# Kernel tuning notes

Hardware: AMD Instinct MI355X
Metric: run time of the kernel (lower is better)

## Reference

```python
import jax, jax.numpy as jnp
import numpy as np

N = 6144       # nodes
E = 12288      # edges (~2N for a sparse simplicial complex)
NF = 32        # node features
EF = 16        # edge features
NH = [32, 32]  # node_hidden
EH = [16, 16]  # edge_hidden
EPS = 1e-5


def setup_inputs() -> dict:
    key = jax.random.key(0)
    ks = jax.random.split(key, 24)
    s = 0.1  # weight init scale
    inp = {}
    inp["X_n"] = jax.random.normal(ks[0], (N, NF), jnp.float32)
    inp["X_e"] = jax.random.normal(ks[1], (E, EF), jnp.float32)
    # normalized adjacency-like operator (non-negative, row mass ~1)
    inp["A_tilde"] = jax.random.uniform(ks[2], (N, N), jnp.float32) * (1.0 / N)
    # normalized Hodge-1 Laplacian-like operator
    inp["L1_tilde"] = jax.random.normal(ks[3], (E, E), jnp.float32) * (1.0 / np.sqrt(E))
    # incidence-like operator
    inp["B1"] = jax.random.normal(ks[4], (N, E), jnp.float32) * (1.0 / np.sqrt(E))
    # GNN linear layers: weight [out, in] (torch convention)
    inp["gnn_W0"] = jax.random.normal(ks[5], (NH[0], NF), jnp.float32) * s
    inp["gnn_b0"] = jnp.zeros((NH[0],), jnp.float32)
    inp["gnn_W1"] = jax.random.normal(ks[6], (NH[1], NH[0]), jnp.float32) * s
    inp["gnn_b1"] = jnp.zeros((NH[1],), jnp.float32)
    # HoSC layer 0: theta in=EF out=EH[0], BN params
    inp["th_W0"] = jax.random.normal(ks[7], (EH[0], EF), jnp.float32) * s
    inp["th_b0"] = jnp.zeros((EH[0],), jnp.float32)
    inp["bn_g0"] = jnp.ones((EH[0],), jnp.float32)
    inp["bn_b0"] = jnp.zeros((EH[0],), jnp.float32)
    # HoSC layer 1: input collapses to 1 channel (max keepdim)
    inp["th_W1"] = jax.random.normal(ks[8], (EH[1], 1), jnp.float32) * s
    inp["th_b1"] = jnp.zeros((EH[1],), jnp.float32)
    inp["bn_g1"] = jnp.ones((EH[1],), jnp.float32)
    inp["bn_b1"] = jnp.zeros((EH[1],), jnp.float32)
    # head: fc1 in = NH[-1] + len(EH) = 34, out = 2N; fc2 out = 1
    inp["fc1_W"] = jax.random.normal(ks[9], (2 * N, NH[-1] + len(EH)), jnp.float32) * s
    inp["fc1_b"] = jnp.zeros((2 * N,), jnp.float32)
    inp["fc2_W"] = jax.random.normal(ks[10], (1, 2 * N), jnp.float32) * s
    inp["fc2_b"] = jnp.zeros((1,), jnp.float32)
    return inp


def _gnn_layer(A, H, W, b):
    # H <- relu((A @ H) @ W^T + b)
    return jax.nn.relu(jnp.matmul(jnp.matmul(A, H), W.T) + b)


def _hosc_layer(Z, L1, W, b, g, beta):
    Zt = jnp.matmul(Z, W.T) + b            # theta
    Zc = jnp.matmul(L1, Zt)                # Laplacian conv
    m = jnp.mean(Zc, axis=0)               # BatchNorm1d (training-mode batch stats)
    v = jnp.var(Zc, axis=0)
    Zp = jax.nn.relu(g * (Zc - m) * jax.lax.rsqrt(v + EPS) + beta)
    return jnp.max(Zp, axis=1, keepdims=True)  # [E, 1]


def reference(X_n, X_e, A_tilde, L1_tilde, B1,
              gnn_W0, gnn_b0, gnn_W1, gnn_b1,
              th_W0, th_b0, bn_g0, bn_b0,
              th_W1, th_b1, bn_g1, bn_b1,
              fc1_W, fc1_b, fc2_W, fc2_b):
    # GNN over nodes
    H = _gnn_layer(A_tilde, X_n, gnn_W0, gnn_b0)
    H_n = _gnn_layer(A_tilde, H, gnn_W1, gnn_b1)      # [N, NH[-1]]
    # HoSC over edges
    Z0 = _hosc_layer(X_e, L1_tilde, th_W0, th_b0, bn_g0, bn_b0)  # [E, 1]
    Z1 = _hosc_layer(Z0, L1_tilde, th_W1, th_b1, bn_g1, bn_b1)   # [E, 1]
    Z_cat = jnp.concatenate([Z0, Z1], axis=1)         # [E, 2]
    H_e = jnp.matmul(B1, Z_cat)                       # [N, 2]
    # head
    Hcat = jnp.concatenate([H_n, H_e], axis=1)        # [N, 34]
    f = jax.nn.relu(jnp.matmul(Hcat, fc1_W.T) + fc1_b)
    f = jnp.matmul(f, fc2_W.T) + fc2_b                # [N, 1]
    return jax.nn.sigmoid(f).squeeze(-1)              # [N]
```

## Files before the change

### kernel.cpp

```cpp
#include <hip/hip_runtime.h>
#include <hip/hip_cooperative_groups.h>
#include <math.h>

namespace cg = cooperative_groups;

#define NND 6144
#define NED 12288
#define GRID 512
static constexpr float EPS_BN = 1e-5f;

#define HN_OFF    0
#define HE_OFF    196608
#define ST_OFF    208896
#define Y_OFF     208960
#define T0_OFF    405568
#define T1_OFF    602176
#define Z0_OFF    798784
#define Z1_OFF    811072
#define U_OFF     823360
#define S_OFF     835648
#define PP_OFF    847936

typedef float floatx4 __attribute__((ext_vector_type(4)));

__device__ __forceinline__ float4 ntload4(const float* p) {
  floatx4 v = __builtin_nontemporal_load(reinterpret_cast<const floatx4*>(p));
  return make_float4(v.x, v.y, v.z, v.w);
}
__device__ __forceinline__ float4 ld4(const float* p) {
  return *reinterpret_cast<const float4*>(p);
}
__device__ __forceinline__ void gll16(const float* g, float* l) {
  __builtin_amdgcn_global_load_lds(
      (const __attribute__((address_space(1))) unsigned int*)g,
      (__attribute__((address_space(3))) unsigned int*)l, 16, 0, 0);
}

struct Params {
  const float *X_n, *X_e, *A, *L1, *B1;
  const float *gW0, *gb0, *gW1, *gb1;
  const float *tW0, *tb0, *bng0, *bnb0;
  const float *tW1, *tb1, *bng1, *bnb1;
  const float *fc1W, *fc1b, *fc2W, *fc2b;
  float *ws;
  float *out;
};

template<int PHASE>
__global__ __launch_bounds__(256, 2) void pipeline(Params p) {
  __shared__ float lds[12288];
  float* sst = &lds[12032];
  float* red = &lds[12064];

  const int tid  = threadIdx.x;
  const int lane = tid & 63;
  const int w    = tid >> 6;
  const int blk  = blockIdx.x;
  const int gtid = blk * 256 + tid;
  constexpr bool ALL = (PHASE == 0);

  float* Hn = p.ws + HN_OFF;
  float* he = p.ws + HE_OFF;
  float* st = p.ws + ST_OFF;
  float* Y  = p.ws + Y_OFF;
  float* T0 = p.ws + T0_OFF;
  float* T1 = p.ws + T1_OFF;
  float* Z0 = p.ws + Z0_OFF;
  float* Z1 = p.ws + Z1_OFF;
  float* u  = p.ws + U_OFF;
  float* s  = p.ws + S_OFF;
  float* pp = p.ws + PP_OFF;

  auto gemm32 = [&](const float* bias, float* outp) {
    const int r0 = blk * 12;
    float acc[3][32];
    #pragma unroll
    for (int r = 0; r < 3; ++r)
      #pragma unroll
      for (int c = 0; c < 32; ++c) acc[r][c] = 0.f;

    for (int kb = 0; kb < NND; kb += 256) {
      #pragma unroll
      for (int i = 0; i < 8; ++i) {
        const int yr = w * 8 + i;
        gll16(Y + (size_t)yr * NND + kb + lane * 4, &lds[yr * 256]);
      }
      #pragma unroll
      for (int i = 0; i < 3; ++i) {
        const int ar = w * 3 + i;
        gll16(p.A + (size_t)(r0 + ar) * NND + kb + lane * 4, &lds[8192 + ar * 256]);
      }
      __syncthreads();
      float4 av[3];
      #pragma unroll
      for (int r = 0; r < 3; ++r)
        av[r] = ld4(&lds[8192 + (w * 3 + r) * 256 + lane * 4]);
      #pragma unroll
      for (int c = 0; c < 32; ++c) {
        const float4 y = ld4(&lds[c * 256 + lane * 4]);
        #pragma unroll
        for (int r = 0; r < 3; ++r) {
          acc[r][c] = fmaf(av[r].x, y.x, acc[r][c]);
          acc[r][c] = fmaf(av[r].y, y.y, acc[r][c]);
          acc[r][c] = fmaf(av[r].z, y.z, acc[r][c]);
          acc[r][c] = fmaf(av[r].w, y.w, acc[r][c]);
        }
      }
      __syncthreads();
    }
    #pragma unroll
    for (int r = 0; r < 3; ++r) {
      float wv[32];
      #pragma unroll
      for (int c = 0; c < 32; ++c)
        wv[c] = acc[r][c] + __shfl_xor(acc[r][c], 32, 64);
      #pragma unroll
      for (int b = 4; b >= 0; --b) {
        const int m = 1 << b;
        const bool hi = (lane & m) != 0;
        #pragma unroll
        for (int i = 0; i < (1 << b); ++i) {
          float x = wv[i], yv = wv[i + (1 << b)];
          float send = hi ? x : yv;
          float recv = __shfl_xor(send, m, 64);
          wv[i] = (hi ? yv : x) + recv;
        }
      }
      if (lane < 32) {
        float v = fmaxf(wv[0] + bias[lane], 0.f);
        outp[(size_t)(r0 + w * 3 + r) * 32 + lane] = v;
      }
    }
  };

  if constexpr (ALL || PHASE == 1) {
    if (blk == 0 && tid < 64) st[tid] = 0.f;
    if (gtid < NND) {
      const int m = gtid;
      float x[32];
      #pragma unroll
      for (int k = 0; k < 32; k += 4) {
        float4 v = ld4(p.X_n + (size_t)m * 32 + k);
        x[k] = v.x; x[k+1] = v.y; x[k+2] = v.z; x[k+3] = v.w;
      }
      #pragma unroll
      for (int oc = 0; oc < 32; ++oc) {
        float acc = 0.f;
        #pragma unroll
        for (int k = 0; k < 32; ++k) acc = fmaf(x[k], p.gW0[oc * 32 + k], acc);
        Y[(size_t)oc * NND + m] = acc;
      }
    } else if (gtid < NND + NED) {
      const int e = gtid - NND;
      float x[16];
      #pragma unroll
      for (int k = 0; k < 16; k += 4) {
        float4 v = ld4(p.X_e + (size_t)e * 16 + k);
        x[k] = v.x; x[k+1] = v.y; x[k+2] = v.z; x[k+3] = v.w;
      }
      #pragma unroll
      for (int oc = 0; oc < 16; ++oc) {
        float acc = p.tb0[oc];
        #pragma unroll
        for (int k = 0; k < 16; ++k) acc = fmaf(x[k], p.tW0[oc * 16 + k], acc);
        T1[(size_t)oc * NED + e] = acc;
      }
    }
  }
  if constexpr (ALL) cg::this_grid().sync();

  if constexpr (ALL || PHASE == 2) gemm32(p.gb0, T0);
  if constexpr (ALL) cg::this_grid().sync();

  if constexpr (ALL || PHASE == 3) {
    if (gtid < NND) {
      const int m = gtid;
      float x[32];
      #pragma unroll
      for (int k = 0; k < 32; k += 4) {
        float4 v = ld4(T0 + (size_t)m * 32 + k);
        x[k] = v.x; x[k+1] = v.y; x[k+2] = v.z; x[k+3] = v.w;
      }
      #pragma unroll
      for (int oc = 0; oc < 32; ++oc) {
        float acc = 0.f;
        #pragma unroll
        for (int k = 0; k < 32; ++k) acc = fmaf(x[k], p.gW1[oc * 32 + k], acc);
        Y[(size_t)oc * NND + m] = acc;
      }
    }
  }
  if constexpr (ALL) cg::this_grid().sync();

  if constexpr (ALL || PHASE == 4) gemm32(p.gb1, Hn);
  if constexpr (ALL) cg::this_grid().sync();

  if constexpr (ALL || PHASE == 5) {
    const int r0 = blk * 24;
    float acc[6][16];
    #pragma unroll
    for (int r = 0; r < 6; ++r)
      #pragma unroll
      for (int c = 0; c < 16; ++c) acc[r][c] = 0.f;

    for (int kb = 0; kb < NED; kb += 256) {
      #pragma unroll
      for (int i = 0; i < 4; ++i) {
        const int yr = w * 4 + i;
        gll16(T1 + (size_t)yr * NED + kb + lane * 4, &lds[yr * 256]);
      }
      #pragma unroll
      for (int i = 0; i < 6; ++i) {
        const int ar = w * 6 + i;
        gll16(p.L1 + (size_t)(r0 + ar) * NED + kb + lane * 4, &lds[4096 + ar * 256]);
      }
      __syncthreads();
      float4 av[6];
      #pragma unroll
      for (int r = 0; r < 6; ++r)
        av[r] = ld4(&lds[4096 + (w * 6 + r) * 256 + lane * 4]);
      #pragma unroll
      for (int c = 0; c < 16; ++c) {
        const float4 y = ld4(&lds[c * 256 + lane * 4]);
        #pragma unroll
        for (int r = 0; r < 6; ++r) {
          acc[r][c] = fmaf(av[r].x, y.x, acc[r][c]);
          acc[r][c] = fmaf(av[r].y, y.y, acc[r][c]);
          acc[r][c] = fmaf(av[r].z, y.z, acc[r][c]);
          acc[r][c] = fmaf(av[r].w, y.w, acc[r][c]);
        }
      }
      __syncthreads();
    }
    float stS = 0.f, stQ = 0.f;
    #pragma unroll
    for (int pr = 0; pr < 3; ++pr) {
      float wv[32];
      #pragma unroll
      for (int c = 0; c < 16; ++c) {
        wv[c]      = acc[2*pr][c]   + __shfl_xor(acc[2*pr][c], 32, 64);
        wv[16 + c] = acc[2*pr+1][c] + __shfl_xor(acc[2*pr+1][c], 32, 64);
      }
      #pragma unroll
      for (int b = 4; b >= 0; --b) {
        const int m = 1 << b;
        const bool hi = (lane & m) != 0;
        #pragma unroll
        for (int i = 0; i < (1 << b); ++i) {
          float x = wv[i], yv = wv[i + (1 << b)];
          float send = hi ? x : yv;
          float recv = __shfl_xor(send, m, 64);
          wv[i] = (hi ? yv : x) + recv;
        }
      }
      if (lane < 32) {
        const int rsel = lane >> 4, csel = lane & 15;
        const float v = wv[0];
        T0[(size_t)(r0 + w * 6 + pr * 2 + rsel) * 16 + csel] = v;
        stS += v; stQ += v * v;
      }
    }
    if (tid < 32) sst[tid] = 0.f;
    __syncthreads();
    if (lane < 32) {
      atomicAdd(&sst[lane & 15], stS);
      atomicAdd(&sst[16 + (lane & 15)], stQ);
    }
    __syncthreads();
    if (tid < 32) atomicAdd(st + tid, sst[tid]);
  }
  if constexpr (ALL) cg::this_grid().sync();

  if constexpr (ALL || PHASE == 6) {
    if (gtid < NED) {
      const int e = gtid;
      const float invE = 1.f / (float)NED;
      float best = -3.4e38f;
      #pragma unroll
      for (int c = 0; c < 16; ++c) {
        float m = st[c] * invE;
        float var = st[16 + c] * invE - m * m;
        float sc = p.bng0[c] * rsqrtf(var + EPS_BN);
        float sh = p.bnb0[c] - m * sc;
        best = fmaxf(best, fmaf(T0[(size_t)e * 16 + c], sc, sh));
      }
      Z0[e] = fmaxf(best, 0.f);
    }
  }
  if constexpr (ALL) cg::this_grid().sync();

  if constexpr (ALL || PHASE == 7) {
    const int rb = GRID - 1 - blk;
    const int r0 = rb * 24 + w * 6;
    const float* mp[6];
    #pragma unroll
    for (int r = 0; r < 6; ++r) mp[r] = p.L1 + (size_t)(r0 + r) * NED;
    float ua[6] = {0,0,0,0,0,0}, sa[6] = {0,0,0,0,0,0};
    float4 a[6], an[6];
    #pragma unroll
    for (int r = 0; r < 6; ++r) a[r] = ntload4(mp[r] + lane * 4);
    float4 z = ld4(Z0 + lane * 4), zn;
    for (int kb = 0; kb < NED; kb += 256) {
      const int k = kb + lane * 4;
      const bool more = (kb + 256) < NED;
      if (more) {
        #pragma unroll
        for (int r = 0; r < 6; ++r) an[r] = ntload4(mp[r] + k + 256);
        zn = ld4(Z0 + k + 256);
      }
      #pragma unroll
      for (int r = 0; r < 6; ++r) {
        ua[r] += a[r].x*z.x + a[r].y*z.y + a[r].z*z.z + a[r].w*z.w;
        sa[r] += a[r].x + a[r].y + a[r].z + a[r].w;
      }
      if (more) {
        #pragma unroll
        for (int r = 0; r < 6; ++r) a[r] = an[r];
        z = zn;
      }
    }
    #pragma unroll
    for (int r = 0; r < 6; ++r)
      #pragma unroll
      for (int m = 1; m < 64; m <<= 1) {
        ua[r] += __shfl_xor(ua[r], m, 64);
        sa[r] += __shfl_xor(sa[r], m, 64);
      }
    if (lane == 0) {
      float s1 = 0.f, s2 = 0.f, s3 = 0.f, s4 = 0.f, s5 = 0.f;
      #pragma unroll
      for (int r = 0; r < 6; ++r) {
        u[r0 + r] = ua[r]; s[r0 + r] = sa[r];
        s1 += ua[r]; s2 += sa[r];
        s3 += ua[r] * ua[r]; s4 += sa[r] * sa[r]; s5 += ua[r] * sa[r];
      }
      red[w * 5 + 0] = s1; red[w * 5 + 1] = s2; red[w * 5 + 2] = s3;
      red[w * 5 + 3] = s4; red[w * 5 + 4] = s5;
    }
    __syncthreads();
    if (tid < 5)
      atomicAdd(st + 32 + tid, red[tid] + red[5 + tid] + red[10 + tid] + red[15 + tid]);
  }
  if constexpr (ALL) cg::this_grid().sync();

  if constexpr (ALL || PHASE == 8) {
    if (gtid < NED) {
      const int e = gtid;
      const float invE = 1.f / (float)NED;
      const float Su = st[32], Ss = st[33], Suu = st[34], Sss = st[35], Sus = st[36];
      const float uu = u[e], ssv = s[e];
      float best = -3.4e38f;
      #pragma unroll
      for (int c = 0; c < 16; ++c) {
        const float wc = p.tW1[c], bc = p.tb1[c];
        const float mean = (wc * Su + bc * Ss) * invE;
        const float ex2 = (wc * wc * Suu + 2.f * wc * bc * Sus + bc * bc * Sss) * invE;
        const float var = ex2 - mean * mean;
        const float sc = p.bng1[c] * rsqrtf(var + EPS_BN);
        const float sh = p.bnb1[c] - mean * sc;
        best = fmaxf(best, fmaf(wc * uu + bc * ssv, sc, sh));
      }
      Z1[e] = fmaxf(best, 0.f);
    }
  }
  if constexpr (ALL) cg::this_grid().sync();

  if constexpr (ALL || PHASE == 9) {
    const int r0 = blk * 12 + w * 3;
    const float* mp[3];
    #pragma unroll
    for (int r = 0; r < 3; ++r) mp[r] = p.B1 + (size_t)(r0 + r) * NED;
    float uu[3] = {0,0,0}, vv[3] = {0,0,0};
    float4 a[3], an[3];
    #pragma unroll
    for (int r = 0; r < 3; ++r) a[r] = ntload4(mp[r] + lane * 4);
    float4 z = ld4(Z0 + lane * 4), y = ld4(Z1 + lane * 4), zn, yn;
    for (int kb = 0; kb < NED; kb += 256) {
      const int k = kb + lane * 4;
      const bool more = (kb + 256) < NED;
      if (more) {
        #pragma unroll
        for (int r = 0; r < 3; ++r) an[r] = ntload4(mp[r] + k + 256);
        zn = ld4(Z0 + k + 256); yn = ld4(Z1 + k + 256);
      }
      #pragma unroll
      for (int r = 0; r < 3; ++r) {
        uu[r] += a[r].x*z.x + a[r].y*z.y + a[r].z*z.z + a[r].w*z.w;
        vv[r] += a[r].x*y.x + a[r].y*y.y + a[r].z*y.z + a[r].w*y.w;
      }
      if (more) {
        #pragma unroll
        for (int r = 0; r < 3; ++r) a[r] = an[r];
        z = zn; y = yn;
      }
    }
    #pragma unroll
    for (int r = 0; r < 3; ++r)
      #pragma unroll
      for (int m = 1; m < 64; m <<= 1) {
        uu[r] += __shfl_xor(uu[r], m, 64);
        vv[r] += __shfl_xor(vv[r], m, 64);
      }
    if (lane == 0) {
      #pragma unroll
      for (int r = 0; r < 3; ++r) {
        he[(r0 + r) * 2]     = uu[r];
        he[(r0 + r) * 2 + 1] = vv[r];
      }
    }
  }
  if constexpr (ALL) cg::this_grid().sync();

  if constexpr (ALL || PHASE == 10) {
    const int nb = blk & 7, jb = blk >> 3;
    int n[3];
    float h[3][34];
    float acc[3] = {0.f, 0.f, 0.f};
    #pragma unroll
    for (int i = 0; i < 3; ++i) {
      n[i] = nb * 768 + i * 256 + tid;
      #pragma unroll
      for (int k = 0; k < 32; k += 4) {
        float4 v = ld4(Hn + (size_t)n[i] * 32 + k);
        h[i][k] = v.x; h[i][k+1] = v.y; h[i][k+2] = v.z; h[i][k+3] = v.w;
      }
      float2 e2 = *reinterpret_cast<const float2*>(he + n[i] * 2);
      h[i][32] = e2.x; h[i][33] = e2.y;
    }
    const int j0 = jb * 192;
    for (int j = j0; j < j0 + 192; ++j) {
      const float* wp = p.fc1W + (size_t)j * 34;
      const float bj = p.fc1b[j], vj = p.fc2W[j];
      float s0 = bj, s1 = bj, s2 = bj;
      #pragma unroll
      for (int k = 0; k < 34; ++k) {
        const float wk = wp[k];
        s0 = fmaf(h[0][k], wk, s0);
        s1 = fmaf(h[1][k], wk, s1);
        s2 = fmaf(h[2][k], wk, s2);
      }
      acc[0] += fmaxf(s0, 0.f) * vj;
      acc[1] += fmaxf(s1, 0.f) * vj;
      acc[2] += fmaxf(s2, 0.f) * vj;
    }
    #pragma unroll
    for (int i = 0; i < 3; ++i) pp[(size_t)jb * NND + n[i]] = acc[i];
  }
  if constexpr (ALL) cg::this_grid().sync();

  if constexpr (ALL || PHASE == 11) {
    if (gtid < NND) {
      float acc = 0.f;
      for (int j = 0; j < 64; ++j) acc += pp[(size_t)j * NND + gtid];
      p.out[gtid] = 1.f / (1.f + expf(-(acc + p.fc2b[0])));
    }
  }
}

extern "C" void kernel_launch(void* const* d_in, const int* in_sizes, int n_in,
                              void* d_out, int out_size, void* d_ws, size_t ws_size,
                              hipStream_t stream) {
  Params p;
  p.X_n  = (const float*)d_in[0];
  p.X_e  = (const float*)d_in[1];
  p.A    = (const float*)d_in[2];
  p.L1   = (const float*)d_in[3];
  p.B1   = (const float*)d_in[4];
  p.gW0  = (const float*)d_in[5];
  p.gb0  = (const float*)d_in[6];
  p.gW1  = (const float*)d_in[7];
  p.gb1  = (const float*)d_in[8];
  p.tW0  = (const float*)d_in[9];
  p.tb0  = (const float*)d_in[10];
  p.bng0 = (const float*)d_in[11];
  p.bnb0 = (const float*)d_in[12];
  p.tW1  = (const float*)d_in[13];
  p.tb1  = (const float*)d_in[14];
  p.bng1 = (const float*)d_in[15];
  p.bnb1 = (const float*)d_in[16];
  p.fc1W = (const float*)d_in[17];
  p.fc1b = (const float*)d_in[18];
  p.fc2W = (const float*)d_in[19];
  p.fc2b = (const float*)d_in[20];
  p.ws   = (float*)d_ws;
  p.out  = (float*)d_out;

  int maxBlk = 0;
  hipError_t oe = hipOccupancyMaxActiveBlocksPerMultiprocessor(
      &maxBlk, pipeline<0>, 256, 0);
  bool coop_ok = (oe == hipSuccess) && (maxBlk >= 2);

  if (coop_ok) {
    void* kargs[] = { &p };
    hipError_t le = hipLaunchCooperativeKernel(
        (const void*)&pipeline<0>, dim3(GRID), dim3(256), kargs, 0, stream);
    if (le == hipSuccess) return;
  }

  pipeline<1><<<GRID, 256, 0, stream>>>(p);
  pipeline<2><<<GRID, 256, 0, stream>>>(p);
  pipeline<3><<<GRID, 256, 0, stream>>>(p);
  pipeline<4><<<GRID, 256, 0, stream>>>(p);
  pipeline<5><<<GRID, 256, 0, stream>>>(p);
  pipeline<6><<<GRID, 256, 0, stream>>>(p);
  pipeline<7><<<GRID, 256, 0, stream>>>(p);
  pipeline<8><<<GRID, 256, 0, stream>>>(p);
  pipeline<9><<<GRID, 256, 0, stream>>>(p);
  pipeline<10><<<GRID, 256, 0, stream>>>(p);
  pipeline<11><<<GRID, 256, 0, stream>>>(p);
}
```

Baseline: 610.3 us.

## Double cooperative grid to 1024 blocks with four blocks per CU

Doubles the cooperative grid and raises the launch bound to four blocks per CU, shrinking LDS per block. Every phase's per-block work is re-split to match: the A GEMM splits columns across wave pairs, the L1 GEMM and row reductions take half the rows, and the head splits fc1 rows into 128 partial chunks. The goal is more waves in flight to hide memory latency in the bandwidth-bound matrix passes. In exchange, accumulators per thread drop to fit the register budget, the A GEMM reloads Y tiles per half-row-set with some idle waves, and the final reduction reads twice as many partial sums.

```diff
diff --git a/kernel.cpp b/kernel.cpp
--- a/kernel.cpp
+++ b/kernel.cpp
@@ -6,7 +6,7 @@
 
 #define NND 6144
 #define NED 12288
-#define GRID 512
+#define GRID 1024
 static constexpr float EPS_BN = 1e-5f;
 
 #define HN_OFF    0
@@ -47,10 +47,10 @@
 };
 
 template<int PHASE>
-__global__ __launch_bounds__(256, 2) void pipeline(Params p) {
-  __shared__ float lds[12288];
-  float* sst = &lds[12032];
-  float* red = &lds[12064];
+__global__ __launch_bounds__(256, 4) void pipeline(Params p) {
+  __shared__ float lds[10240];
+  float* sst = &lds[10176];
+  float* red = &lds[10208];
 
   const int tid  = threadIdx.x;
   const int lane = tid & 63;
@@ -72,12 +72,14 @@
   float* pp = p.ws + PP_OFF;
 
   auto gemm32 = [&](const float* bias, float* outp) {
-    const int r0 = blk * 12;
-    float acc[3][32];
+    const int rg = w >> 1, cg_ = w & 1;
+    const int r0 = blk * 6;
+    const int c0 = cg_ * 16;
+    float acc[3][16];
     #pragma unroll
     for (int r = 0; r < 3; ++r)
       #pragma unroll
-      for (int c = 0; c < 32; ++c) acc[r][c] = 0.f;
+      for (int c = 0; c < 16; ++c) acc[r][c] = 0.f;
 
     for (int kb = 0; kb < NND; kb += 256) {
       #pragma unroll
@@ -86,18 +88,19 @@
         gll16(Y + (size_t)yr * NND + kb + lane * 4, &lds[yr * 256]);
       }
       #pragma unroll
-      for (int i = 0; i < 3; ++i) {
-        const int ar = w * 3 + i;
-        gll16(p.A + (size_t)(r0 + ar) * NND + kb + lane * 4, &lds[8192 + ar * 256]);
+      for (int i = 0; i < 2; ++i) {
+        const int ar = w * 2 + i;
+        if (ar < 6)
+          gll16(p.A + (size_t)(r0 + ar) * NND + kb + lane * 4, &lds[8192 + ar * 256]);
       }
       __syncthreads();
       float4 av[3];
       #pragma unroll
       for (int r = 0; r < 3; ++r)
-        av[r] = ld4(&lds[8192 + (w * 3 + r) * 256 + lane * 4]);
-      #pragma unroll
-      for (int c = 0; c < 32; ++c) {
-        const float4 y = ld4(&lds[c * 256 + lane * 4]);
+        av[r] = ld4(&lds[8192 + (rg * 3 + r) * 256 + lane * 4]);
+      #pragma unroll
+      for (int c = 0; c < 16; ++c) {
+        const float4 y = ld4(&lds[(c0 + c) * 256 + lane * 4]);
         #pragma unroll
         for (int r = 0; r < 3; ++r) {
           acc[r][c] = fmaf(av[r].x, y.x, acc[r][c]);
@@ -110,12 +113,14 @@
     }
     #pragma unroll
     for (int r = 0; r < 3; ++r) {
-      float wv[32];
-      #pragma unroll
-      for (int c = 0; c < 32; ++c)
-        wv[c] = acc[r][c] + __shfl_xor(acc[r][c], 32, 64);
-      #pragma unroll
-      for (int b = 4; b >= 0; --b) {
+      float wv[16];
+      #pragma unroll
+      for (int c = 0; c < 16; ++c) {
+        float t = acc[r][c] + __shfl_xor(acc[r][c], 32, 64);
+        wv[c] = t + __shfl_xor(t, 16, 64);
+      }
+      #pragma unroll
+      for (int b = 3; b >= 0; --b) {
         const int m = 1 << b;
         const bool hi = (lane & m) != 0;
         #pragma unroll
@@ -126,9 +131,9 @@
           wv[i] = (hi ? yv : x) + recv;
         }
       }
-      if (lane < 32) {
-        float v = fmaxf(wv[0] + bias[lane], 0.f);
-        outp[(size_t)(r0 + w * 3 + r) * 32 + lane] = v;
+      if (lane < 16) {
+        float v = fmaxf(wv[0] + bias[c0 + lane], 0.f);
+        outp[(size_t)(r0 + rg * 3 + r) * 32 + c0 + lane] = v;
       }
     }
   };
@@ -196,10 +201,10 @@
   if constexpr (ALL) cg::this_grid().sync();
 
   if constexpr (ALL || PHASE == 5) {
-    const int r0 = blk * 24;
-    float acc[6][16];
-    #pragma unroll
-    for (int r = 0; r < 6; ++r)
+    const int r0 = blk * 12;
+    float acc[3][16];
+    #pragma unroll
+    for (int r = 0; r < 3; ++r)
       #pragma unroll
       for (int c = 0; c < 16; ++c) acc[r][c] = 0.f;
 
@@ -210,20 +215,20 @@
         gll16(T1 + (size_t)yr * NED + kb + lane * 4, &lds[yr * 256]);
       }
       #pragma unroll
-      for (int i = 0; i < 6; ++i) {
-        const int ar = w * 6 + i;
+      for (int i = 0; i < 3; ++i) {
+        const int ar = w * 3 + i;
         gll16(p.L1 + (size_t)(r0 + ar) * NED + kb + lane * 4, &lds[4096 + ar * 256]);
       }
       __syncthreads();
-      float4 av[6];
-      #pragma unroll
-      for (int r = 0; r < 6; ++r)
-        av[r] = ld4(&lds[4096 + (w * 6 + r) * 256 + lane * 4]);
+      float4 av[3];
+      #pragma unroll
+      for (int r = 0; r < 3; ++r)
+        av[r] = ld4(&lds[4096 + (w * 3 + r) * 256 + lane * 4]);
       #pragma unroll
       for (int c = 0; c < 16; ++c) {
         const float4 y = ld4(&lds[c * 256 + lane * 4]);
         #pragma unroll
-        for (int r = 0; r < 6; ++r) {
+        for (int r = 0; r < 3; ++r) {
           acc[r][c] = fmaf(av[r].x, y.x, acc[r][c]);
           acc[r][c] = fmaf(av[r].y, y.y, acc[r][c]);
           acc[r][c] = fmaf(av[r].z, y.z, acc[r][c]);
@@ -234,15 +239,15 @@
     }
     float stS = 0.f, stQ = 0.f;
     #pragma unroll
-    for (int pr = 0; pr < 3; ++pr) {
-      float wv[32];
+    for (int r = 0; r < 3; ++r) {
+      float wv[16];
       #pragma unroll
       for (int c = 0; c < 16; ++c) {
-        wv[c]      = acc[2*pr][c]   + __shfl_xor(acc[2*pr][c], 32, 64);
-        wv[16 + c] = acc[2*pr+1][c] + __shfl_xor(acc[2*pr+1][c], 32, 64);
-      }
-      #pragma unroll
-      for (int b = 4; b >= 0; --b) {
+        float t = acc[r][c] + __shfl_xor(acc[r][c], 32, 64);
+        wv[c] = t + __shfl_xor(t, 16, 64);
+      }
+      #pragma unroll
+      for (int b = 3; b >= 0; --b) {
         const int m = 1 << b;
         const bool hi = (lane & m) != 0;
         #pragma unroll
@@ -253,18 +258,17 @@
           wv[i] = (hi ? yv : x) + recv;
         }
       }
-      if (lane < 32) {
-        const int rsel = lane >> 4, csel = lane & 15;
+      if (lane < 16) {
         const float v = wv[0];
-        T0[(size_t)(r0 + w * 6 + pr * 2 + rsel) * 16 + csel] = v;
+        T0[(size_t)(r0 + w * 3 + r) * 16 + lane] = v;
         stS += v; stQ += v * v;
       }
     }
     if (tid < 32) sst[tid] = 0.f;
     __syncthreads();
-    if (lane < 32) {
-      atomicAdd(&sst[lane & 15], stS);
-      atomicAdd(&sst[16 + (lane & 15)], stQ);
+    if (lane < 16) {
+      atomicAdd(&sst[lane], stS);
+      atomicAdd(&sst[16 + lane], stQ);
     }
     __syncthreads();
     if (tid < 32) atomicAdd(st + tid, sst[tid]);
@@ -291,36 +295,36 @@
 
   if constexpr (ALL || PHASE == 7) {
     const int rb = GRID - 1 - blk;
-    const int r0 = rb * 24 + w * 6;
-    const float* mp[6];
-    #pragma unroll
-    for (int r = 0; r < 6; ++r) mp[r] = p.L1 + (size_t)(r0 + r) * NED;
-    float ua[6] = {0,0,0,0,0,0}, sa[6] = {0,0,0,0,0,0};
-    float4 a[6], an[6];
-    #pragma unroll
-    for (int r = 0; r < 6; ++r) a[r] = ntload4(mp[r] + lane * 4);
+    const int r0 = rb * 12 + w * 3;
+    const float* mp[3];
+    #pragma unroll
+    for (int r = 0; r < 3; ++r) mp[r] = p.L1 + (size_t)(r0 + r) * NED;
+    float ua[3] = {0,0,0}, sa[3] = {0,0,0};
+    float4 a[3], an[3];
+    #pragma unroll
+    for (int r = 0; r < 3; ++r) a[r] = ntload4(mp[r] + lane * 4);
     float4 z = ld4(Z0 + lane * 4), zn;
     for (int kb = 0; kb < NED; kb += 256) {
       const int k = kb + lane * 4;
       const bool more = (kb + 256) < NED;
       if (more) {
         #pragma unroll
-        for (int r = 0; r < 6; ++r) an[r] = ntload4(mp[r] + k + 256);
+        for (int r = 0; r < 3; ++r) an[r] = ntload4(mp[r] + k + 256);
         zn = ld4(Z0 + k + 256);
       }
       #pragma unroll
-      for (int r = 0; r < 6; ++r) {
+      for (int r = 0; r < 3; ++r) {
         ua[r] += a[r].x*z.x + a[r].y*z.y + a[r].z*z.z + a[r].w*z.w;
         sa[r] += a[r].x + a[r].y + a[r].z + a[r].w;
       }
       if (more) {
         #pragma unroll
-        for (int r = 0; r < 6; ++r) a[r] = an[r];
+        for (int r = 0; r < 3; ++r) a[r] = an[r];
         z = zn;
       }
     }
     #pragma unroll
-    for (int r = 0; r < 6; ++r)
+    for (int r = 0; r < 3; ++r)
       #pragma unroll
       for (int m = 1; m < 64; m <<= 1) {
         ua[r] += __shfl_xor(ua[r], m, 64);
@@ -329,7 +333,7 @@
     if (lane == 0) {
       float s1 = 0.f, s2 = 0.f, s3 = 0.f, s4 = 0.f, s5 = 0.f;
       #pragma unroll
-      for (int r = 0; r < 6; ++r) {
+      for (int r = 0; r < 3; ++r) {
         u[r0 + r] = ua[r]; s[r0 + r] = sa[r];
         s1 += ua[r]; s2 += sa[r];
         s3 += ua[r] * ua[r]; s4 += sa[r] * sa[r]; s5 += ua[r] * sa[r];
@@ -367,45 +371,47 @@
 
   if constexpr (ALL || PHASE == 9) {
     const int r0 = blk * 12 + w * 3;
-    const float* mp[3];
-    #pragma unroll
-    for (int r = 0; r < 3; ++r) mp[r] = p.B1 + (size_t)(r0 + r) * NED;
-    float uu[3] = {0,0,0}, vv[3] = {0,0,0};
-    float4 a[3], an[3];
-    #pragma unroll
-    for (int r = 0; r < 3; ++r) a[r] = ntload4(mp[r] + lane * 4);
-    float4 z = ld4(Z0 + lane * 4), y = ld4(Z1 + lane * 4), zn, yn;
-    for (int kb = 0; kb < NED; kb += 256) {
-      const int k = kb + lane * 4;
-      const bool more = (kb + 256) < NED;
-      if (more) {
-        #pragma unroll
-        for (int r = 0; r < 3; ++r) an[r] = ntload4(mp[r] + k + 256);
-        zn = ld4(Z0 + k + 256); yn = ld4(Z1 + k + 256);
-      }
-      #pragma unroll
-      for (int r = 0; r < 3; ++r) {
-        uu[r] += a[r].x*z.x + a[r].y*z.y + a[r].z*z.z + a[r].w*z.w;
-        vv[r] += a[r].x*y.x + a[r].y*y.y + a[r].z*y.z + a[r].w*y.w;
-      }
-      if (more) {
-        #pragma unroll
-        for (int r = 0; r < 3; ++r) a[r] = an[r];
-        z = zn; y = yn;
-      }
-    }
-    #pragma unroll
-    for (int r = 0; r < 3; ++r)
-      #pragma unroll
-      for (int m = 1; m < 64; m <<= 1) {
-        uu[r] += __shfl_xor(uu[r], m, 64);
-        vv[r] += __shfl_xor(vv[r], m, 64);
-      }
-    if (lane == 0) {
-      #pragma unroll
-      for (int r = 0; r < 3; ++r) {
-        he[(r0 + r) * 2]     = uu[r];
-        he[(r0 + r) * 2 + 1] = vv[r];
+    if (r0 < NND) {
+      const float* mp[3];
+      #pragma unroll
+      for (int r = 0; r < 3; ++r) mp[r] = p.B1 + (size_t)(r0 + r) * NED;
+      float uu[3] = {0,0,0}, vv[3] = {0,0,0};
+      float4 a[3], an[3];
+      #pragma unroll
+      for (int r = 0; r < 3; ++r) a[r] = ntload4(mp[r] + lane * 4);
+      float4 z = ld4(Z0 + lane * 4), y = ld4(Z1 + lane * 4), zn, yn;
+      for (int kb = 0; kb < NED; kb += 256) {
+        const int k = kb + lane * 4;
+        const bool more = (kb + 256) < NED;
+        if (more) {
+          #pragma unroll
+          for (int r = 0; r < 3; ++r) an[r] = ntload4(mp[r] + k + 256);
+          zn = ld4(Z0 + k + 256); yn = ld4(Z1 + k + 256);
+        }
+        #pragma unroll
+        for (int r = 0; r < 3; ++r) {
+          uu[r] += a[r].x*z.x + a[r].y*z.y + a[r].z*z.z + a[r].w*z.w;
+          vv[r] += a[r].x*y.x + a[r].y*y.y + a[r].z*y.z + a[r].w*y.w;
+        }
+        if (more) {
+          #pragma unroll
+          for (int r = 0; r < 3; ++r) a[r] = an[r];
+          z = zn; y = yn;
+        }
+      }
+      #pragma unroll
+      for (int r = 0; r < 3; ++r)
+        #pragma unroll
+        for (int m = 1; m < 64; m <<= 1) {
+          uu[r] += __shfl_xor(uu[r], m, 64);
+          vv[r] += __shfl_xor(vv[r], m, 64);
+        }
+      if (lane == 0) {
+        #pragma unroll
+        for (int r = 0; r < 3; ++r) {
+          he[(r0 + r) * 2]     = uu[r];
+          he[(r0 + r) * 2 + 1] = vv[r];
+        }
       }
     }
   }
@@ -427,8 +433,8 @@
       float2 e2 = *reinterpret_cast<const float2*>(he + n[i] * 2);
       h[i][32] = e2.x; h[i][33] = e2.y;
     }
-    const int j0 = jb * 192;
-    for (int j = j0; j < j0 + 192; ++j) {
+    const int j0 = jb * 96;
+    for (int j = j0; j < j0 + 96; ++j) {
       const float* wp = p.fc1W + (size_t)j * 34;
       const float bj = p.fc1b[j], vj = p.fc2W[j];
       float s0 = bj, s1 = bj, s2 = bj;
@@ -451,7 +457,7 @@
   if constexpr (ALL || PHASE == 11) {
     if (gtid < NND) {
       float acc = 0.f;
-      for (int j = 0; j < 64; ++j) acc += pp[(size_t)j * NND + gtid];
+      for (int j = 0; j < 128; ++j) acc += pp[(size_t)j * NND + gtid];
       p.out[gtid] = 1.f / (1.f + expf(-(acc + p.fc2b[0])));
     }
   }
@@ -488,7 +494,7 @@
   int maxBlk = 0;
   hipError_t oe = hipOccupancyMaxActiveBlocksPerMultiprocessor(
       &maxBlk, pipeline<0>, 256, 0);
-  bool coop_ok = (oe == hipSuccess) && (maxBlk >= 2);
+  bool coop_ok = (oe == hipSuccess) && (maxBlk >= 4);
 
   if (coop_ok) {
     void* kargs[] = { &p };
```

Measured after the change: 578.3 us. 5.2% less time.
